# Kernel tuning notes

Measured on AMD Instinct MI355X. Metric: run time of the kernel, lower is better.

## Reference

```python
import jax, jax.numpy as jnp
import numpy as np

N, E = 100000, 1600000
F_IN, H, C = 64, 64, 40


def setup_inputs() -> dict:
    key = jax.random.key(0)
    k = jax.random.split(key, 6)
    x = jax.random.normal(k[0], (N, F_IN), jnp.float32)
    edge_index = jax.random.randint(k[1], (2, E), 0, N, jnp.int32)
    edge_weight = jax.random.uniform(k[2], (E,), jnp.float32)
    W1 = jax.random.normal(k[3], (F_IN, H), jnp.float32) / np.sqrt(F_IN)
    b1 = jnp.zeros((H,), jnp.float32)
    W2 = jax.random.normal(k[4], (H, C), jnp.float32) / np.sqrt(H)
    b2 = jnp.zeros((C,), jnp.float32)
    return {"x": x, "edge_index": edge_index, "edge_weight": edge_weight,
            "W1": W1, "b1": b1, "W2": W2, "b2": b2}


def reference(x, edge_index, edge_weight, W1, b1, W2, b2):
    # PyG GCNConv: add self-loops (weight 1), symmetric normalization
    # D^{-1/2} (A + I) D^{-1/2}, linear transform, scatter-add, bias.
    n = x.shape[0]
    src, dst = edge_index[0], edge_index[1]
    loop = jnp.arange(n, dtype=src.dtype)
    src_f = jnp.concatenate([src, loop])
    dst_f = jnp.concatenate([dst, loop])
    w_f = jnp.concatenate([edge_weight, jnp.ones((n,), edge_weight.dtype)])
    deg = jax.ops.segment_sum(w_f, dst_f, num_segments=n)
    dinv = jnp.where(deg > 0, jax.lax.rsqrt(deg), 0.0)
    norm = dinv[src_f] * w_f * dinv[dst_f]  # [E+N]

    def conv(h, W, b):
        h = h @ W                                    # [n, d_out]
        msg = h[src_f] * norm[:, None]               # gather + scale, [E+N, d_out]
        return jax.ops.segment_sum(msg, dst_f, num_segments=n) + b

    h = jax.nn.relu(conv(x, W1, b1))
    # dropout is identity in eval mode (training=False)
    h = conv(h, W2, b2)
    return jax.nn.log_softmax(h, axis=1)
```

## Files before the change

kernel.cpp:

```cpp
#include <hip/hip_runtime.h>
#include <math.h>

#define N_NODES 100000
#define N_EDGES 1600000
#define C_DIM 40
#define NGROUPS 6250

#define BSZ 256
#define NB  ((N_NODES + BSZ - 1) / BSZ)
#define EB  4096
#define NBE ((N_EDGES + EB - 1) / EB)

#define OFF_DINV 0
#define OFF_BB   100000
#define OFF_CS   100392
#define OFF_ROW  100800
#define OFF_H    200802
#define OFF_REC2 353684
#define OFF_H1P  3553684
#define OFF_H2P  6753684
#define OFF_R1P  9953684

typedef float floatx4 __attribute__((ext_vector_type(4)));
typedef short shortx8 __attribute__((ext_vector_type(8)));

__device__ inline unsigned short f2bf(float f) {
    unsigned int u = __float_as_uint(f);
    u += 0x7FFF + ((u >> 16) & 1);
    return (unsigned short)(u >> 16);
}
__device__ inline float bf2f(unsigned short h) {
    return __uint_as_float(((unsigned int)h) << 16);
}
__device__ inline float bflo(unsigned int u) { return __uint_as_float(u << 16); }
__device__ inline float bfhi(unsigned int u) { return __uint_as_float(u & 0xFFFF0000u); }

__global__ __launch_bounds__(512) void k_hist2d(const int* __restrict__ ei,
                                                int* __restrict__ H,
                                                int* __restrict__ colsum) {
    __shared__ int bins[NB];
    int t = threadIdx.x, b = blockIdx.x;
    for (int i = t; i < NB; i += 512) bins[i] = 0;
    __syncthreads();
    int base = b * EB;
    for (int i = t; i < EB; i += 512) {
        int e = base + i;
        if (e < N_EDGES) atomicAdd(&bins[ei[N_EDGES + e] >> 8], 1);
    }
    __syncthreads();
    for (int i = t; i < NB; i += 512) {
        int c = bins[i];
        H[b * NB + i] = c;
        if (c) atomicAdd(&colsum[i], c);
    }
}

__global__ __launch_bounds__(512) void k_colscan(int* __restrict__ H,
                                                 const int* __restrict__ colsum,
                                                 int* __restrict__ bucketBase,
                                                 int* __restrict__ rowStart) {
    __shared__ int sd[512];
    __shared__ int sbase;
    int t = threadIdx.x, j = blockIdx.x;
    int p = 0;
    for (int i = t; i < j; i += 512) p += colsum[i];
    sd[t] = p;
    __syncthreads();
    for (int off = 256; off > 0; off >>= 1) {
        if (t < off) sd[t] += sd[t + off];
        __syncthreads();
    }
    if (t == 0) sbase = sd[0];
    __syncthreads();
    int base = sbase;
    if (t == 0) {
        bucketBase[j] = base;
        if (j == NB - 1) { bucketBase[NB] = base + colsum[j]; rowStart[N_NODES] = N_EDGES; }
    }
    __syncthreads();
    int val = (t < NBE) ? H[t * NB + j] : 0;
    sd[t] = val;
    __syncthreads();
    for (int off = 1; off < 512; off <<= 1) {
        int v = (t >= off) ? sd[t - off] : 0;
        __syncthreads();
        sd[t] += v;
        __syncthreads();
    }
    if (t < NBE) H[t * NB + j] = base + sd[t] - val;
}

__global__ __launch_bounds__(512) void k_scatter(const int* __restrict__ ei,
                                                 const float* __restrict__ w,
                                                 const int* __restrict__ blockBase,
                                                 int2* __restrict__ rec) {
    __shared__ int bases[NB];
    __shared__ int cur[NB];
    int t = threadIdx.x, b = blockIdx.x;
    for (int i = t; i < NB; i += 512) { bases[i] = blockBase[b * NB + i]; cur[i] = 0; }
    __syncthreads();
    int base = b * EB;
    for (int i = t; i < EB; i += 512) {
        int e = base + i;
        if (e < N_EDGES) {
            int s = ei[e], d = ei[N_EDGES + e];
            float wv = w[e];
            int bin = d >> 8;
            int pos = bases[bin] + atomicAdd(&cur[bin], 1);
            rec[pos] = make_int2(s | ((d & 255) << 17), __float_as_int(wv));
        }
    }
}

__global__ __launch_bounds__(512) void k_bsort(const int* __restrict__ bucketBase,
                                               const int2* __restrict__ rec,
                                               int2* __restrict__ rec2,
                                               float* __restrict__ dinv,
                                               int* __restrict__ rowStart) {
    __shared__ int   cnt[256];
    __shared__ float wsum[256];
    __shared__ int   cur[256];
    __shared__ int   sd[512];
    int t = threadIdx.x, b = blockIdx.x;
    if (t < 256) { cnt[t] = 0; wsum[t] = 0.f; }
    __syncthreads();
    int r0 = bucketBase[b], r1 = bucketBase[b + 1];
    for (int i = r0 + t; i < r1; i += 512) {
        int2 rv = rec[i];
        int l = (rv.x >> 17) & 255;
        atomicAdd(&cnt[l], 1);
        atomicAdd(&wsum[l], __int_as_float(rv.y));
    }
    __syncthreads();
    int val = (t < 256) ? cnt[t] : 0;
    sd[t] = val;
    __syncthreads();
    for (int off = 1; off < 512; off <<= 1) {
        int v = (t >= off) ? sd[t - off] : 0;
        __syncthreads();
        sd[t] += v;
        __syncthreads();
    }
    float dloc = 0.f;
    if (t < 256) {
        int excl = sd[t] - val;
        cur[t] = excl;
        int node = b * BSZ + t;
        dloc = rsqrtf(1.f + wsum[t]);
        if (node < N_NODES) {
            rowStart[node] = r0 + excl;
            dinv[node] = dloc;
        }
    }
    __syncthreads();
    if (t < 256) wsum[t] = dloc;
    __syncthreads();
    for (int i = r0 + t; i < r1; i += 512) {
        int2 rv = rec[i];
        int l = (rv.x >> 17) & 255;
        float cpart = __int_as_float(rv.y) * wsum[l];
        int pos = r0 + atomicAdd(&cur[l], 1);
        rec2[pos] = make_int2((rv.x & 0x1FFFF) << 7, __float_as_int(cpart));
    }
}

__global__ __launch_bounds__(256) void k_mm1(const float* __restrict__ x,
                                             const float* __restrict__ W1,
                                             const float* __restrict__ dinv,
                                             unsigned short* __restrict__ h1p) {
    int t = threadIdx.x, lane = t & 63, wv = t >> 6;
    int m = lane & 15, quad = lane >> 4;
    int wid = blockIdx.x * 4 + wv, nw = gridDim.x * 4;
    shortx8 B[2][4];
#pragma unroll
    for (int kc = 0; kc < 2; ++kc)
#pragma unroll
        for (int tt = 0; tt < 4; ++tt)
#pragma unroll
            for (int j = 0; j < 8; ++j) {
                int k = kc * 32 + quad * 8 + j;
                B[kc][tt][j] = (short)f2bf(W1[k * 64 + tt * 16 + m]);
            }
    for (int g = wid; g < NGROUPS; g += nw) {
        int n0 = g * 16;
        const float* xr = x + (long)(n0 + m) * 64 + quad * 8;
        floatx4 xa = ((const floatx4*)xr)[0];
        floatx4 xb = ((const floatx4*)(xr + 4))[0];
        floatx4 xc = ((const floatx4*)(xr + 32))[0];
        floatx4 xd = ((const floatx4*)(xr + 36))[0];
        shortx8 A0, A1;
#pragma unroll
        for (int j = 0; j < 4; ++j) {
            A0[j] = (short)f2bf(xa[j]);
            A0[4 + j] = (short)f2bf(xb[j]);
            A1[j] = (short)f2bf(xc[j]);
            A1[4 + j] = (short)f2bf(xd[j]);
        }
        floatx4 acc[4];
#pragma unroll
        for (int tt = 0; tt < 4; ++tt) {
            acc[tt] = (floatx4){0.f, 0.f, 0.f, 0.f};
            acc[tt] = __builtin_amdgcn_mfma_f32_16x16x32_bf16(A0, B[0][tt], acc[tt], 0, 0, 0);
            acc[tt] = __builtin_amdgcn_mfma_f32_16x16x32_bf16(A1, B[1][tt], acc[tt], 0, 0, 0);
        }
        floatx4 dv = ((const floatx4*)(dinv + n0 + quad * 4))[0];
#pragma unroll
        for (int reg = 0; reg < 4; ++reg) {
            int node = n0 + quad * 4 + reg;
            float d = dv[reg];
#pragma unroll
            for (int tt = 0; tt < 4; ++tt)
                h1p[(long)node * 64 + tt * 16 + m] = f2bf(acc[tt][reg] * d);
        }
    }
}

__global__ __launch_bounds__(256) void k_agg1(const int* __restrict__ rowStart,
                                              const int2* __restrict__ rec2,
                                              const float* __restrict__ dinv,
                                              const unsigned short* __restrict__ h1p,
                                              const float* __restrict__ b1,
                                              unsigned short* __restrict__ r1p) {
    __shared__ int2 cache[4][64];
    int t = threadIdx.x, lane = t & 63, wv = t >> 6;
    int node = blockIdx.x * 4 + wv;
    if (node >= N_NODES) return;
    int2* wc = cache[wv];
    wc[lane] = make_int2(0, 0);
    const char* hb = (const char*)h1p;
    int eslot = lane >> 3;
    int c = lane & 7;
    int lo = c << 4;
    float dn = dinv[node];
    float a0 = 0, a1 = 0, a2 = 0, a3 = 0, a4 = 0, a5 = 0, a6 = 0, a7 = 0;
    float g0 = 0, g1 = 0, g2 = 0, g3 = 0, g4 = 0, g5 = 0, g6 = 0, g7 = 0;
    if (eslot == 0) {
        uint4 u = *(const uint4*)(hb + ((long)node << 7) + lo);
        a0 = bflo(u.x) * dn; a1 = bfhi(u.x) * dn;
        a2 = bflo(u.y) * dn; a3 = bfhi(u.y) * dn;
        a4 = bflo(u.z) * dn; a5 = bfhi(u.z) * dn;
        a6 = bflo(u.w) * dn; a7 = bfhi(u.w) * dn;
    }
    int s0 = rowStart[node], s1 = rowStart[node + 1];
    for (int base = s0; base < s1; base += 64) {
        int idx = base + lane;
        if (idx < s1) wc[lane] = rec2[idx];
        __builtin_amdgcn_wave_barrier();
        int cnt = min(64, s1 - base);
        int j = 0;
        for (; j + 15 < cnt; j += 16) {
            int2 eA = wc[j + eslot];
            int2 eB = wc[j + 8 + eslot];
            uint4 uA = *(const uint4*)(hb + eA.x + lo);
            uint4 uB = *(const uint4*)(hb + eB.x + lo);
            float cA = __int_as_float(eA.y), cB = __int_as_float(eB.y);
            a0 = fmaf(bflo(uA.x), cA, a0); a1 = fmaf(bfhi(uA.x), cA, a1);
            a2 = fmaf(bflo(uA.y), cA, a2); a3 = fmaf(bfhi(uA.y), cA, a3);
            a4 = fmaf(bflo(uA.z), cA, a4); a5 = fmaf(bfhi(uA.z), cA, a5);
            a6 = fmaf(bflo(uA.w), cA, a6); a7 = fmaf(bfhi(uA.w), cA, a7);
            g0 = fmaf(bflo(uB.x), cB, g0); g1 = fmaf(bfhi(uB.x), cB, g1);
            g2 = fmaf(bflo(uB.y), cB, g2); g3 = fmaf(bfhi(uB.y), cB, g3);
            g4 = fmaf(bflo(uB.z), cB, g4); g5 = fmaf(bfhi(uB.z), cB, g5);
            g6 = fmaf(bflo(uB.w), cB, g6); g7 = fmaf(bfhi(uB.w), cB, g7);
        }
        for (; j < cnt; j += 8) {
            int jj = j + eslot;
            bool valid = jj < cnt;
            int2 e = wc[valid ? jj : j];
            float cc = valid ? __int_as_float(e.y) : 0.f;
            uint4 u = *(const uint4*)(hb + e.x + lo);
            a0 = fmaf(bflo(u.x), cc, a0); a1 = fmaf(bfhi(u.x), cc, a1);
            a2 = fmaf(bflo(u.y), cc, a2); a3 = fmaf(bfhi(u.y), cc, a3);
            a4 = fmaf(bflo(u.z), cc, a4); a5 = fmaf(bfhi(u.z), cc, a5);
            a6 = fmaf(bflo(u.w), cc, a6); a7 = fmaf(bfhi(u.w), cc, a7);
        }
        __builtin_amdgcn_wave_barrier();
    }
    a0 += g0; a1 += g1; a2 += g2; a3 += g3;
    a4 += g4; a5 += g5; a6 += g6; a7 += g7;
#define RED(v) v += __shfl_xor(v, 8, 64); v += __shfl_xor(v, 16, 64); v += __shfl_xor(v, 32, 64)
    RED(a0); RED(a1); RED(a2); RED(a3); RED(a4); RED(a5); RED(a6); RED(a7);
#undef RED
    if (eslot == 0) {
        floatx4 bva = ((const floatx4*)(b1 + (c << 3)))[0];
        floatx4 bvb = ((const floatx4*)(b1 + (c << 3) + 4))[0];
        shortx8 v;
        v[0] = (short)f2bf(fmaxf(a0 + bva[0], 0.f));
        v[1] = (short)f2bf(fmaxf(a1 + bva[1], 0.f));
        v[2] = (short)f2bf(fmaxf(a2 + bva[2], 0.f));
        v[3] = (short)f2bf(fmaxf(a3 + bva[3], 0.f));
        v[4] = (short)f2bf(fmaxf(a4 + bvb[0], 0.f));
        v[5] = (short)f2bf(fmaxf(a5 + bvb[1], 0.f));
        v[6] = (short)f2bf(fmaxf(a6 + bvb[2], 0.f));
        v[7] = (short)f2bf(fmaxf(a7 + bvb[3], 0.f));
        *(shortx8*)(r1p + ((long)node << 6) + (c << 3)) = v;
    }
}

__global__ __launch_bounds__(256) void k_mm2(const unsigned short* __restrict__ r1p,
                                             const float* __restrict__ W2,
                                             const float* __restrict__ dinv,
                                             unsigned short* __restrict__ h2p) {
    int t = threadIdx.x, lane = t & 63, wv = t >> 6;
    int m = lane & 15, quad = lane >> 4;
    int wid = blockIdx.x * 4 + wv, nw = gridDim.x * 4;
    shortx8 B[2][3];
#pragma unroll
    for (int kc = 0; kc < 2; ++kc)
#pragma unroll
        for (int tt = 0; tt < 3; ++tt) {
            int n = tt * 16 + m;
#pragma unroll
            for (int j = 0; j < 8; ++j) {
                int k = kc * 32 + quad * 8 + j;
                B[kc][tt][j] = (n < C_DIM) ? (short)f2bf(W2[k * C_DIM + n]) : (short)0;
            }
        }
    for (int g = wid; g < NGROUPS; g += nw) {
        int n0 = g * 16;
        const unsigned short* rr = r1p + ((long)(n0 + m) << 6) + quad * 8;
        shortx8 A0 = *(const shortx8*)rr;
        shortx8 A1 = *(const shortx8*)(rr + 32);
        floatx4 acc[3];
#pragma unroll
        for (int tt = 0; tt < 3; ++tt) {
            acc[tt] = (floatx4){0.f, 0.f, 0.f, 0.f};
            acc[tt] = __builtin_amdgcn_mfma_f32_16x16x32_bf16(A0, B[0][tt], acc[tt], 0, 0, 0);
            acc[tt] = __builtin_amdgcn_mfma_f32_16x16x32_bf16(A1, B[1][tt], acc[tt], 0, 0, 0);
        }
        floatx4 dv = ((const floatx4*)(dinv + n0 + quad * 4))[0];
#pragma unroll
        for (int reg = 0; reg < 4; ++reg) {
            int node = n0 + quad * 4 + reg;
            float d = dv[reg];
#pragma unroll
            for (int tt = 0; tt < 3; ++tt) {
                int col = tt * 16 + m;
                if (col < C_DIM)
                    h2p[((long)node << 6) + col] = f2bf(acc[tt][reg] * d);
            }
        }
    }
}

__global__ __launch_bounds__(256) void k_agg2(const int* __restrict__ rowStart,
                                              const int2* __restrict__ rec2,
                                              const float* __restrict__ dinv,
                                              const unsigned short* __restrict__ h2p,
                                              const float* __restrict__ b2,
                                              float* __restrict__ out) {
    __shared__ int2 cache[4][64];
    int t = threadIdx.x, lane = t & 63, wv = t >> 6;
    int node = blockIdx.x * 4 + wv;
    if (node >= N_NODES) return;
    int2* wc = cache[wv];
    wc[lane] = make_int2(0, 0);
    const char* hb = (const char*)h2p;
    int eslot = lane / 10;
    int c = lane - eslot * 10;
    bool elane = eslot < 6;
    int lo = c << 3;
    float dn = dinv[node];
    float a0 = 0, a1 = 0, a2 = 0, a3 = 0;
    float g0 = 0, g1 = 0, g2 = 0, g3 = 0;
    if (eslot == 0) {
        uint2 u = *(const uint2*)(hb + ((long)node << 7) + lo);
        a0 = bflo(u.x) * dn; a1 = bfhi(u.x) * dn;
        a2 = bflo(u.y) * dn; a3 = bfhi(u.y) * dn;
    }
    int s0 = rowStart[node], s1 = rowStart[node + 1];
    for (int base = s0; base < s1; base += 64) {
        int idx = base + lane;
        if (idx < s1) wc[lane] = rec2[idx];
        __builtin_amdgcn_wave_barrier();
        int cnt = min(64, s1 - base);
        int j = 0;
        for (; j + 11 < cnt; j += 12) {
            int2 eA = wc[j + eslot];
            int2 eB = wc[j + 6 + eslot];
            uint2 uA = *(const uint2*)(hb + eA.x + lo);
            uint2 uB = *(const uint2*)(hb + eB.x + lo);
            float cA = elane ? __int_as_float(eA.y) : 0.f;
            float cB = elane ? __int_as_float(eB.y) : 0.f;
            a0 = fmaf(bflo(uA.x), cA, a0); a1 = fmaf(bfhi(uA.x), cA, a1);
            a2 = fmaf(bflo(uA.y), cA, a2); a3 = fmaf(bfhi(uA.y), cA, a3);
            g0 = fmaf(bflo(uB.x), cB, g0); g1 = fmaf(bfhi(uB.x), cB, g1);
            g2 = fmaf(bflo(uB.y), cB, g2); g3 = fmaf(bfhi(uB.y), cB, g3);
        }
        for (; j < cnt; j += 6) {
            int jj = j + eslot;
            bool valid = elane && (jj < cnt);
            int2 e = wc[valid ? jj : j];
            float cc = valid ? __int_as_float(e.y) : 0.f;
            uint2 u = *(const uint2*)(hb + e.x + lo);
            a0 = fmaf(bflo(u.x), cc, a0); a1 = fmaf(bfhi(u.x), cc, a1);
            a2 = fmaf(bflo(u.y), cc, a2); a3 = fmaf(bfhi(u.y), cc, a3);
        }
        __builtin_amdgcn_wave_barrier();
    }
    a0 += g0; a1 += g1; a2 += g2; a3 += g3;
#define RED6(v) v += __shfl(v, (lane + 30) & 63, 64); \
                v += __shfl(v, (lane + 10) & 63, 64) + __shfl(v, (lane + 20) & 63, 64)
    RED6(a0); RED6(a1); RED6(a2); RED6(a3);
#undef RED6
    bool act = lane < 10;
    floatx4 bb = act ? ((const floatx4*)(b2 + (c << 2)))[0] : (floatx4){0, 0, 0, 0};
    float v0 = act ? a0 + bb[0] : -INFINITY;
    float v1 = act ? a1 + bb[1] : -INFINITY;
    float v2 = act ? a2 + bb[2] : -INFINITY;
    float v3 = act ? a3 + bb[3] : -INFINITY;
    float m = fmaxf(fmaxf(v0, v1), fmaxf(v2, v3));
#pragma unroll
    for (int off = 32; off; off >>= 1) m = fmaxf(m, __shfl_xor(m, off, 64));
    float s = act ? (expf(v0 - m) + expf(v1 - m)) + (expf(v2 - m) + expf(v3 - m)) : 0.f;
#pragma unroll
    for (int off = 32; off; off >>= 1) s += __shfl_xor(s, off, 64);
    float ls = m + logf(s);
    if (act) {
        *(float4*)(out + (long)node * C_DIM + (c << 2)) =
            make_float4(v0 - ls, v1 - ls, v2 - ls, v3 - ls);
    }
}

extern "C" void kernel_launch(void* const* d_in, const int* in_sizes, int n_in,
                              void* d_out, int out_size, void* d_ws, size_t ws_size,
                              hipStream_t stream) {
    const float* x  = (const float*)d_in[0];
    const int*   ei = (const int*)d_in[1];
    const float* w  = (const float*)d_in[2];
    const float* W1 = (const float*)d_in[3];
    const float* b1 = (const float*)d_in[4];
    const float* W2 = (const float*)d_in[5];
    const float* b2 = (const float*)d_in[6];
    float* out = (float*)d_out;

    float* wsf = (float*)d_ws;
    int*   wsi = (int*)d_ws;
    float* dinv       = wsf + OFF_DINV;
    int*   bucketBase = wsi + OFF_BB;
    int*   colsum     = wsi + OFF_CS;
    int*   rowStart   = wsi + OFF_ROW;
    int*   H          = wsi + OFF_H;
    int2*  rec2       = (int2*)(wsi + OFF_REC2);
    int2*  rec        = (int2*)(wsi + OFF_H1P);
    unsigned short* h1p = (unsigned short*)(wsi + OFF_H1P);
    unsigned short* h2p = (unsigned short*)(wsi + OFF_H2P);
    unsigned short* r1p = (unsigned short*)(wsi + OFF_R1P);

    hipMemsetAsync(colsum, 0, NB * sizeof(int), stream);
    k_hist2d<<<NBE, 512, 0, stream>>>(ei, H, colsum);
    k_colscan<<<NB, 512, 0, stream>>>(H, colsum, bucketBase, rowStart);
    k_scatter<<<NBE, 512, 0, stream>>>(ei, w, H, rec);
    k_bsort<<<NB, 512, 0, stream>>>(bucketBase, rec, rec2, dinv, rowStart);

    k_mm1<<<512, 256, 0, stream>>>(x, W1, dinv, h1p);
    k_agg1<<<(N_NODES + 3) / 4, 256, 0, stream>>>(rowStart, rec2, dinv, h1p, b1, r1p);

    k_mm2<<<512, 256, 0, stream>>>(r1p, W2, dinv, h2p);
    k_agg2<<<(N_NODES + 3) / 4, 256, 0, stream>>>(rowStart, rec2, dinv, h2p, b2, out);
}
```

Measured before the change: 280.4 us.

## Fuse CSR build kernels into one persistent kernel with grid barriers

```diff
diff --git a/kernel.cpp b/kernel.cpp
--- a/kernel.cpp
+++ b/kernel.cpp
@@ -14,6 +14,7 @@
 #define OFF_DINV 0
 #define OFF_BB   100000
 #define OFF_CS   100392
+#define OFF_BAR  100784
 #define OFF_ROW  100800
 #define OFF_H    200802
 #define OFF_REC2 353684
@@ -29,39 +30,60 @@
     u += 0x7FFF + ((u >> 16) & 1);
     return (unsigned short)(u >> 16);
 }
-__device__ inline float bf2f(unsigned short h) {
-    return __uint_as_float(((unsigned int)h) << 16);
-}
 __device__ inline float bflo(unsigned int u) { return __uint_as_float(u << 16); }
 __device__ inline float bfhi(unsigned int u) { return __uint_as_float(u & 0xFFFF0000u); }
 
-__global__ __launch_bounds__(512) void k_hist2d(const int* __restrict__ ei,
-                                                int* __restrict__ H,
-                                                int* __restrict__ colsum) {
-    __shared__ int bins[NB];
-    int t = threadIdx.x, b = blockIdx.x;
+__device__ __forceinline__ void gbar(int* bar, int nb) {
+    __syncthreads();
+    if (threadIdx.x == 0) {
+        __threadfence();
+        __hip_atomic_fetch_add(bar, 1, __ATOMIC_RELEASE, __HIP_MEMORY_SCOPE_AGENT);
+        while (__hip_atomic_load(bar, __ATOMIC_ACQUIRE, __HIP_MEMORY_SCOPE_AGENT) < nb)
+            __builtin_amdgcn_s_sleep(1);
+        __threadfence();
+    }
+    __syncthreads();
+}
+
+__global__ __launch_bounds__(512) void k_build(const int* __restrict__ ei,
+                                               const float* __restrict__ w,
+                                               int* __restrict__ H,
+                                               int* __restrict__ colsum,
+                                               int* __restrict__ bucketBase,
+                                               int* __restrict__ rowStart,
+                                               int2* __restrict__ rec,
+                                               int2* __restrict__ rec2,
+                                               float* __restrict__ dinv,
+                                               int* bar) {
+    __shared__ int   sd[512];
+    __shared__ int   sbase;
+    __shared__ int   bins[NB];
+    __shared__ int   cur[NB];
+    __shared__ float wsum[256];
+    int t = threadIdx.x, b = blockIdx.x, nb = gridDim.x;
+    int base = b * EB;
+
     for (int i = t; i < NB; i += 512) bins[i] = 0;
     __syncthreads();
-    int base = b * EB;
     for (int i = t; i < EB; i += 512) {
         int e = base + i;
         if (e < N_EDGES) atomicAdd(&bins[ei[N_EDGES + e] >> 8], 1);
     }
     __syncthreads();
-    for (int i = t; i < NB; i += 512) {
-        int c = bins[i];
-        H[b * NB + i] = c;
-        if (c) atomicAdd(&colsum[i], c);
-    }
-}
-
-__global__ __launch_bounds__(512) void k_colscan(int* __restrict__ H,
-                                                 const int* __restrict__ colsum,
-                                                 int* __restrict__ bucketBase,
-                                                 int* __restrict__ rowStart) {
-    __shared__ int sd[512];
-    __shared__ int sbase;
-    int t = threadIdx.x, j = blockIdx.x;
+    for (int i = t; i < NB; i += 512) H[b * NB + i] = bins[i];
+    gbar(bar + 0, nb);
+
+    int j = b;
+    int val = (t < NBE) ? H[t * NB + j] : 0;
+    sd[t] = val;
+    __syncthreads();
+    for (int off = 256; off > 0; off >>= 1) {
+        if (t < off) sd[t] += sd[t + off];
+        __syncthreads();
+    }
+    if (t == 0) colsum[j] = sd[0];
+    gbar(bar + 1, nb);
+
     int p = 0;
     for (int i = t; i < j; i += 512) p += colsum[i];
     sd[t] = p;
@@ -72,13 +94,12 @@
     }
     if (t == 0) sbase = sd[0];
     __syncthreads();
-    int base = sbase;
+    int cbase = sbase;
     if (t == 0) {
-        bucketBase[j] = base;
-        if (j == NB - 1) { bucketBase[NB] = base + colsum[j]; rowStart[N_NODES] = N_EDGES; }
-    }
-    __syncthreads();
-    int val = (t < NBE) ? H[t * NB + j] : 0;
+        bucketBase[j] = cbase;
+        if (j == NB - 1) { bucketBase[NB] = cbase + colsum[j]; rowStart[N_NODES] = N_EDGES; }
+    }
+    __syncthreads();
     sd[t] = val;
     __syncthreads();
     for (int off = 1; off < 512; off <<= 1) {
@@ -87,63 +108,45 @@
         sd[t] += v;
         __syncthreads();
     }
-    if (t < NBE) H[t * NB + j] = base + sd[t] - val;
-}
-
-__global__ __launch_bounds__(512) void k_scatter(const int* __restrict__ ei,
-                                                 const float* __restrict__ w,
-                                                 const int* __restrict__ blockBase,
-                                                 int2* __restrict__ rec) {
-    __shared__ int bases[NB];
-    __shared__ int cur[NB];
-    int t = threadIdx.x, b = blockIdx.x;
-    for (int i = t; i < NB; i += 512) { bases[i] = blockBase[b * NB + i]; cur[i] = 0; }
-    __syncthreads();
-    int base = b * EB;
+    if (t < NBE) H[t * NB + j] = cbase + sd[t] - val;
+    gbar(bar + 2, nb);
+
+    for (int i = t; i < NB; i += 512) { bins[i] = H[b * NB + i]; cur[i] = 0; }
+    __syncthreads();
     for (int i = t; i < EB; i += 512) {
         int e = base + i;
         if (e < N_EDGES) {
             int s = ei[e], d = ei[N_EDGES + e];
             float wv = w[e];
             int bin = d >> 8;
-            int pos = bases[bin] + atomicAdd(&cur[bin], 1);
+            int pos = bins[bin] + atomicAdd(&cur[bin], 1);
             rec[pos] = make_int2(s | ((d & 255) << 17), __float_as_int(wv));
         }
     }
-}
-
-__global__ __launch_bounds__(512) void k_bsort(const int* __restrict__ bucketBase,
-                                               const int2* __restrict__ rec,
-                                               int2* __restrict__ rec2,
-                                               float* __restrict__ dinv,
-                                               int* __restrict__ rowStart) {
-    __shared__ int   cnt[256];
-    __shared__ float wsum[256];
-    __shared__ int   cur[256];
-    __shared__ int   sd[512];
-    int t = threadIdx.x, b = blockIdx.x;
-    if (t < 256) { cnt[t] = 0; wsum[t] = 0.f; }
+    gbar(bar + 3, nb);
+
+    if (t < 256) { bins[t] = 0; wsum[t] = 0.f; }
     __syncthreads();
     int r0 = bucketBase[b], r1 = bucketBase[b + 1];
     for (int i = r0 + t; i < r1; i += 512) {
         int2 rv = rec[i];
         int l = (rv.x >> 17) & 255;
-        atomicAdd(&cnt[l], 1);
+        atomicAdd(&bins[l], 1);
         atomicAdd(&wsum[l], __int_as_float(rv.y));
     }
     __syncthreads();
-    int val = (t < 256) ? cnt[t] : 0;
-    sd[t] = val;
+    int v4 = (t < 256) ? bins[t] : 0;
+    sd[t] = v4;
     __syncthreads();
     for (int off = 1; off < 512; off <<= 1) {
-        int v = (t >= off) ? sd[t - off] : 0;
-        __syncthreads();
-        sd[t] += v;
+        int u = (t >= off) ? sd[t - off] : 0;
+        __syncthreads();
+        sd[t] += u;
         __syncthreads();
     }
     float dloc = 0.f;
     if (t < 256) {
-        int excl = sd[t] - val;
+        int excl = sd[t] - v4;
         cur[t] = excl;
         int node = b * BSZ + t;
         dloc = rsqrtf(1.f + wsum[t]);
@@ -177,9 +180,9 @@
 #pragma unroll
         for (int tt = 0; tt < 4; ++tt)
 #pragma unroll
-            for (int j = 0; j < 8; ++j) {
-                int k = kc * 32 + quad * 8 + j;
-                B[kc][tt][j] = (short)f2bf(W1[k * 64 + tt * 16 + m]);
+            for (int jj = 0; jj < 8; ++jj) {
+                int k = kc * 32 + quad * 8 + jj;
+                B[kc][tt][jj] = (short)f2bf(W1[k * 64 + tt * 16 + m]);
             }
     for (int g = wid; g < NGROUPS; g += nw) {
         int n0 = g * 16;
@@ -190,11 +193,11 @@
         floatx4 xd = ((const floatx4*)(xr + 36))[0];
         shortx8 A0, A1;
 #pragma unroll
-        for (int j = 0; j < 4; ++j) {
-            A0[j] = (short)f2bf(xa[j]);
-            A0[4 + j] = (short)f2bf(xb[j]);
-            A1[j] = (short)f2bf(xc[j]);
-            A1[4 + j] = (short)f2bf(xd[j]);
+        for (int jj = 0; jj < 4; ++jj) {
+            A0[jj] = (short)f2bf(xa[jj]);
+            A0[4 + jj] = (short)f2bf(xb[jj]);
+            A1[jj] = (short)f2bf(xc[jj]);
+            A1[4 + jj] = (short)f2bf(xd[jj]);
         }
         floatx4 acc[4];
 #pragma unroll
@@ -311,9 +314,9 @@
         for (int tt = 0; tt < 3; ++tt) {
             int n = tt * 16 + m;
 #pragma unroll
-            for (int j = 0; j < 8; ++j) {
-                int k = kc * 32 + quad * 8 + j;
-                B[kc][tt][j] = (n < C_DIM) ? (short)f2bf(W2[k * C_DIM + n]) : (short)0;
+            for (int jj = 0; jj < 8; ++jj) {
+                int k = kc * 32 + quad * 8 + jj;
+                B[kc][tt][jj] = (n < C_DIM) ? (short)f2bf(W2[k * C_DIM + n]) : (short)0;
             }
         }
     for (int g = wid; g < NGROUPS; g += nw) {
@@ -439,6 +442,7 @@
     float* dinv       = wsf + OFF_DINV;
     int*   bucketBase = wsi + OFF_BB;
     int*   colsum     = wsi + OFF_CS;
+    int*   bar        = wsi + OFF_BAR;
     int*   rowStart   = wsi + OFF_ROW;
     int*   H          = wsi + OFF_H;
     int2*  rec2       = (int2*)(wsi + OFF_REC2);
@@ -447,15 +451,13 @@
     unsigned short* h2p = (unsigned short*)(wsi + OFF_H2P);
     unsigned short* r1p = (unsigned short*)(wsi + OFF_R1P);
 
-    hipMemsetAsync(colsum, 0, NB * sizeof(int), stream);
-    k_hist2d<<<NBE, 512, 0, stream>>>(ei, H, colsum);
-    k_colscan<<<NB, 512, 0, stream>>>(H, colsum, bucketBase, rowStart);
-    k_scatter<<<NBE, 512, 0, stream>>>(ei, w, H, rec);
-    k_bsort<<<NB, 512, 0, stream>>>(bucketBase, rec, rec2, dinv, rowStart);
-
-    k_mm1<<<512, 256, 0, stream>>>(x, W1, dinv, h1p);
+    hipMemsetAsync(bar, 0, 4 * sizeof(int), stream);
+    k_build<<<NB, 512, 0, stream>>>(ei, w, H, colsum, bucketBase, rowStart,
+                                    rec, rec2, dinv, bar);
+
+    k_mm1<<<1024, 256, 0, stream>>>(x, W1, dinv, h1p);
     k_agg1<<<(N_NODES + 3) / 4, 256, 0, stream>>>(rowStart, rec2, dinv, h1p, b1, r1p);
 
-    k_mm2<<<512, 256, 0, stream>>>(r1p, W2, dinv, h2p);
+    k_mm2<<<1024, 256, 0, stream>>>(r1p, W2, dinv, h2p);
     k_agg2<<<(N_NODES + 3) / 4, 256, 0, stream>>>(rowStart, rec2, dinv, h2p, b2, out);
 }
```

Result: slower. 537.1 us (+91.5%).
